# Optimization experiments

Measured on AMD Instinct MI355X. Metric: run time of the kernel, lower is better.

## Reference

```python
import jax, jax.numpy as jnp
import numpy as np

SOS_TOKEN = 0


def setup_inputs() -> dict:
    B, T, V, E, H = 128, 512, 1024, 256, 512
    key = jax.random.key(0)
    ks = jax.random.split(key, 11)
    return {
        "encoder_outputs": jax.random.normal(ks[0], (B, 8, H), jnp.float32),
        "enc_h": jax.random.normal(ks[1], (2, B, H), jnp.float32),
        "enc_c": jax.random.normal(ks[2], (2, B, H), jnp.float32),
        "target_tensor": jax.random.randint(ks[3], (B, T), 0, V, jnp.int64 if jax.config.jax_enable_x64 else jnp.int32),
        "embedding": jax.random.normal(ks[4], (V, E), jnp.float32) * 0.02,
        "W_ih": jax.random.normal(ks[5], (4 * H, E), jnp.float32) * 0.05,
        "W_hh": jax.random.normal(ks[6], (4 * H, H), jnp.float32) * 0.05,
        "b_ih": jax.random.normal(ks[7], (4 * H,), jnp.float32) * 0.05,
        "b_hh": jax.random.normal(ks[8], (4 * H,), jnp.float32) * 0.05,
        "W_out": jax.random.normal(ks[9], (V, H), jnp.float32) * 0.05,
        "b_out": jax.random.normal(ks[10], (V,), jnp.float32) * 0.05,
    }


def reference(encoder_outputs, enc_h, enc_c, target_tensor, embedding,
              W_ih, W_hh, b_ih, b_hh, W_out, b_out):
    B = encoder_outputs.shape[0]
    H = W_hh.shape[1]
    # decoder initial state: mean over encoder layer dim -> (B, H)
    h0 = enc_h.mean(axis=0)
    c0 = enc_c.mean(axis=0)
    # teacher-forced input tokens: [SOS, y_0, ..., y_{T-2}]  -> (B, T)
    sos = jnp.full((B, 1), SOS_TOKEN, dtype=target_tensor.dtype)
    tokens = jnp.concatenate([sos, target_tensor[:, :-1]], axis=1)
    # embed + relu, then precompute all input-side gate projections: (B, T, 4H)
    x = jax.nn.relu(embedding[tokens])
    gates_x = jnp.einsum("bte,ge->btg", x, W_ih) + b_ih + b_hh

    def lstm_step(carry, gx):
        h, c = carry  # (B, H) each; gx: (B, 4H)
        gates = gx + h @ W_hh.T
        i, f, g, o = jnp.split(gates, 4, axis=-1)  # torch gate order i,f,g,o
        c = jax.nn.sigmoid(f) * c + jax.nn.sigmoid(i) * jnp.tanh(g)
        h = jax.nn.sigmoid(o) * jnp.tanh(c)
        return (h, c), h

    (h_T, c_T), hs = jax.lax.scan(lstm_step, (h0, c0), gates_x.transpose(1, 0, 2))
    hs = hs.transpose(1, 0, 2)  # (B, T, H)
    logits = jnp.einsum("bth,vh->btv", hs, W_out) + b_out
    log_probs = jax.nn.log_softmax(logits, axis=-1)
    # final hidden mirrors torch's (num_layers=1, B, H) layout
    return log_probs, h_T[None], c_T[None]
```

## Files before the change

### kernel.cpp

```cpp
#include <hip/hip_runtime.h>

typedef unsigned short u16;
typedef unsigned int u32;
typedef unsigned long long u64;
typedef short bf16x8 __attribute__((ext_vector_type(8)));
typedef float f32x4 __attribute__((ext_vector_type(4)));
typedef unsigned u32x4 __attribute__((ext_vector_type(4)));

#define NB 128
#define NT 512
#define NV 1024
#define NE 256
#define NH 512
#define NG 2048

#define POISON64 0xFFFFFFFFFFFFFFFFULL
#define POISON32 0xFFFFFFFFu
#define HEX_T 65536
#define PROBE_CYCLES 480000ULL

__device__ __forceinline__ u16 f2bf(float f) {
  union { float f; unsigned u; } v; v.f = f;
  unsigned r = v.u + 0x7FFFu + ((v.u >> 16) & 1u);
  return (u16)(r >> 16);
}
__device__ __forceinline__ float bf2f(u16 u) {
  union { unsigned u; float f; } v; v.u = ((unsigned)u) << 16;
  return v.f;
}
__device__ __forceinline__ float sigm(float x) { return 1.f / (1.f + __expf(-x)); }
__device__ __forceinline__ float tanh_f(float x) {
  x = fminf(fmaxf(x, -20.f), 20.f);
  float e = __expf(2.f * x);
  return (e - 1.f) / (e + 1.f);
}
__device__ __forceinline__ u64 memtime() {
  u64 t;
  asm volatile("s_memtime %0\n\ts_waitcnt lgkmcnt(0)" : "=s"(t));
  return t;
}

#define MFMA16(a, b, c) __builtin_amdgcn_mfma_f32_16x16x32_bf16((a), (b), (c), 0, 0, 0)

__device__ __forceinline__ uint2 pf_load_u64(const void* p) {
  uint2 r;
  asm volatile("global_load_dwordx2 %0, %1, off" : "=v"(r) : "v"(p) : "memory");
  return r;
}
__device__ __forceinline__ void ex_store(u16* p, u64 v) {
  (void)__hip_atomic_exchange((u64*)p, v, __ATOMIC_RELAXED, __HIP_MEMORY_SCOPE_AGENT);
}
__device__ __forceinline__ void ex_load2(const u16* p, bool fast, u32x4& q0, u32x4& q1) {
  if (fast) {
    asm volatile(
        "global_load_dwordx4 %0, %2, off sc0\n\t"
        "global_load_dwordx4 %1, %3, off sc0\n\t"
        "s_waitcnt vmcnt(0)"
        : "=&v"(q0), "=&v"(q1)
        : "v"(p), "v"(p + 8)
        : "memory");
  } else {
    asm volatile(
        "global_load_dwordx4 %0, %2, off sc0 sc1\n\t"
        "global_load_dwordx4 %1, %3, off sc0 sc1\n\t"
        "s_waitcnt vmcnt(0)"
        : "=&v"(q0), "=&v"(q1)
        : "v"(p), "v"(p + 8)
        : "memory");
  }
}

__device__ __forceinline__ void stage_h(const u16* hexg, u16* HsBuf, int tid, bool fast) {
  const u16* p = hexg + (size_t)tid * 16;
  u32x4 q0, q1;
  ex_load2(p, fast, q0, q1);
  for (;;) {
    u64 a = (u64)q0.x | ((u64)q0.y << 32), b = (u64)q0.z | ((u64)q0.w << 32);
    u64 c = (u64)q1.x | ((u64)q1.y << 32), d = (u64)q1.z | ((u64)q1.w << 32);
    if (!((a == POISON64) | (b == POISON64) | (c == POISON64) | (d == POISON64))) break;
    ex_load2(p, fast, q0, q1);
  }
  int s2 = tid >> 5, b = (tid >> 1) & 15, half = tid & 1;
  int K0 = s2 * 4 + half * 2;
  *(u32x4*)&HsBuf[b * 512 + ((K0 ^ (b & 7)) << 3)] = q0;
  *(u32x4*)&HsBuf[b * 512 + (((K0 + 1) ^ (b & 7)) << 3)] = q1;
}

__device__ __forceinline__ void group_setup(u32* ctrl, u32* disc_lds, int* fast_shp,
                                            int bid, int tid, int& g, int& s, bool& fast) {
  u32* disc = ctrl; u32* probe = ctrl + 128; u32* ready2 = ctrl + 256; u32* demote = ctrl + 384;
  int w = tid >> 6, lane = tid & 63;
  if (tid == 0) {
    u32 xcd;
    asm volatile("s_getreg_b32 %0, hwreg(HW_REG_XCC_ID)" : "=s"(xcd));
    __hip_atomic_store(&disc[bid], xcd & 7u, __ATOMIC_RELAXED, __HIP_MEMORY_SCOPE_AGENT);
  }
  if (w == 0) {
    const u64* d64 = (const u64*)disc;
    u64 v;
    do { v = __hip_atomic_load(&d64[lane], __ATOMIC_RELAXED, __HIP_MEMORY_SCOPE_AGENT); }
    while ((u32)v == POISON32 || (u32)(v >> 32) == POISON32);
    disc_lds[2 * lane] = (u32)v; disc_lds[2 * lane + 1] = (u32)(v >> 32);
  }
  __syncthreads();
  u64 cnt64 = 0;
  for (int i = 0; i < 128; ++i) cnt64 += 1ULL << ((disc_lds[i] & 7) * 8);
  int myx = (int)(disc_lds[bid] & 7);
  int rank = 0;
  for (int i = 0; i < bid; ++i) if ((int)(disc_lds[i] & 7) == myx) rank++;
  int pre = 0;
  for (int x = 0; x < myx; ++x) pre += (int)((cnt64 >> (x * 8)) & 255);
  int pos = pre + rank;
  g = pos >> 4; s = pos & 15;
  fast = false;
  { int p0 = 0;
    for (int x = 0; x < 8; ++x) { int c = (int)((cnt64 >> (x * 8)) & 255);
      if (p0 <= g * 16 && g * 16 + 16 <= p0 + c) fast = true; p0 += c; } }
  if (fast) {
    if (tid == 0)
      (void)__hip_atomic_exchange(&probe[g * 16 + s], 1u, __ATOMIC_RELAXED,
                                  __HIP_MEMORY_SCOPE_AGENT);
    if (w == 0) {
      bool to = false;
      if (lane < 16) {
        u32 pv = POISON32;
        u64 t0 = memtime();
        for (;;) {
          asm volatile("global_load_dword %0, %1, off sc0\n\ts_waitcnt vmcnt(0)"
                       : "=v"(pv) : "v"(&probe[g * 16 + lane]) : "memory");
          if (pv != POISON32) break;
          if (memtime() - t0 > PROBE_CYCLES) break;
        }
        to = (pv == POISON32);
      }
      if (__any(to) && lane == 0) {
        __hip_atomic_store(&demote[g], 1u, __ATOMIC_RELAXED, __HIP_MEMORY_SCOPE_AGENT);
        asm volatile("s_waitcnt vmcnt(0)" ::: "memory");
      }
    }
    __syncthreads();
    if (tid == 0)
      __hip_atomic_store(&ready2[g * 16 + s], 1u, __ATOMIC_RELAXED, __HIP_MEMORY_SCOPE_AGENT);
    if (w == 0 && lane < 16) {
      u32 rv;
      do { rv = __hip_atomic_load(&ready2[g * 16 + lane], __ATOMIC_RELAXED, __HIP_MEMORY_SCOPE_AGENT); }
      while (rv == POISON32);
    }
    if (tid == 0)
      *fast_shp = (int)(__hip_atomic_load(&demote[g], __ATOMIC_RELAXED, __HIP_MEMORY_SCOPE_AGENT) == 0u);
    __syncthreads();
    fast = (*fast_shp != 0);
  }
}

__global__ __launch_bounds__(256) void prep_kernel(
    const float* __restrict__ enc_h, const float* __restrict__ W_ih,
    const float* __restrict__ W_hh, const float* __restrict__ b_ih,
    const float* __restrict__ b_hh, const float* __restrict__ W_out,
    u16* __restrict__ wih_p, u16* __restrict__ whh_p, u16* __restrict__ wout_b,
    float* __restrict__ bias_p, u16* __restrict__ hex, u32* __restrict__ ctrl) {
  int idx = blockIdx.x * 256 + threadIdx.x;
  int stride = gridDim.x * 256;
  if (idx < 128) { ctrl[idx] = POISON32; ctrl[128 + idx] = POISON32; ctrl[256 + idx] = POISON32; }
  if (idx < 8) ctrl[384 + idx] = 0;
  const int N0 = NG * NE, N1 = NG * NH, N2 = NV * NH, N3 = NG, N4 = NB * NH;
  int total = N0 + N1 + N2 + N3 + N4;
  for (int i = idx; i < total; i += stride) {
    int j = i;
    if (j < N0) {
      int r = j >> 8, k = j & 255;
      int orig = (r & 3) * NH + (r >> 2);
      wih_p[j] = f2bf(W_ih[orig * NE + k]);
    } else if ((j -= N0) < N1) {
      int r = j >> 9, k = j & 511;
      int orig = (r & 3) * NH + (r >> 2);
      whh_p[j] = f2bf(W_hh[orig * NH + k]);
    } else if ((j -= N1) < N2) {
      wout_b[j] = f2bf(W_out[j]);
    } else if ((j -= N2) < N3) {
      int orig = (j & 3) * NH + (j >> 2);
      bias_p[j] = b_ih[orig] + b_hh[orig];
    } else {
      j -= N3;
      int bb = j >> 9, jj = j & 511;
      float v = 0.5f * (enc_h[j] + enc_h[N4 + j]);
      hex[((size_t)(bb >> 4) * 16 + (jj >> 5)) * 512 + (size_t)(bb & 15) * 32 + (jj & 31)] = f2bf(v);
    }
  }
  u64* hp = (u64*)(hex + HEX_T);
  const int NP = NT * (HEX_T / 4);
  for (int i = idx; i < NP; i += stride) hp[i] = POISON64;
}

__global__ __launch_bounds__(256) void gates_kernel(
    const int* __restrict__ target, const float* __restrict__ emb,
    const u16* __restrict__ wih_p, const float* __restrict__ bias_p,
    u16* __restrict__ gates) {
  __shared__ __align__(16) u16 As[NB * NE];
  int t = blockIdx.y, nTile = blockIdx.x, tid = threadIdx.x;
  for (int i = tid; i < NB * 64; i += 256) {
    int row = i >> 6, c = i & 63;
    int tok = (t == 0) ? 0 : target[row * NT + t - 1];
    float4 f = *(const float4*)(emb + (size_t)tok * NE + c * 4);
    ushort4 pk = make_ushort4(f2bf(fmaxf(f.x, 0.f)), f2bf(fmaxf(f.y, 0.f)),
                              f2bf(fmaxf(f.z, 0.f)), f2bf(fmaxf(f.w, 0.f)));
    int g = c >> 1;
    int off = row * NE + ((((g ^ (row & 7)) << 3)) | ((c & 1) << 2));
    *(ushort4*)&As[off] = pk;
  }
  __syncthreads();
  int w = tid >> 6, lane = tid & 63, l15 = lane & 15, l4 = lane >> 4;
  int mOff = (w & 1) * 64, nOff = (w >> 1) * 64;
  f32x4 acc[4][4] = {};
  for (int kk = 0; kk < 8; ++kk) {
    bf16x8 a[4], bb[4];
    for (int fm = 0; fm < 4; ++fm) {
      int row = mOff + fm * 16 + l15;
      a[fm] = *(const bf16x8*)&As[row * NE + (((kk * 4 + l4) ^ (row & 7)) << 3)];
    }
    int k0 = kk * 32 + l4 * 8;
    for (int fn = 0; fn < 4; ++fn) {
      int n = nTile * 128 + nOff + fn * 16 + l15;
      bb[fn] = *(const bf16x8*)(wih_p + (size_t)n * NE + k0);
    }
    for (int fm = 0; fm < 4; ++fm)
      for (int fn = 0; fn < 4; ++fn)
        acc[fm][fn] = MFMA16(a[fm], bb[fn], acc[fm][fn]);
  }
  for (int fn = 0; fn < 4; ++fn) {
    int n = nTile * 128 + nOff + fn * 16 + l15;
    float bias = bias_p[n];
    for (int fm = 0; fm < 4; ++fm)
      for (int i2 = 0; i2 < 4; ++i2) {
        int row = mOff + fm * 16 + l4 * 4 + i2;
        gates[((size_t)t * NB + row) * NG + n] = f2bf(acc[fm][fn][i2] + bias);
      }
  }
}

__global__ __launch_bounds__(512, 1) void lstm_kernel(
    const float* __restrict__ enc_c, const u16* __restrict__ gates,
    const u16* __restrict__ whh_p, u16* __restrict__ hex,
    float* __restrict__ out_tail, u32* __restrict__ ctrl) {
  __shared__ __align__(16) u16 Hs[2][16 * 512];
  __shared__ u32 disc_lds[128];
  __shared__ int fast_sh;
  int bid = blockIdx.x, tid = threadIdx.x;
  int w = tid >> 6, lane = tid & 63, l15 = lane & 15, l4 = lane >> 4;
  int g, s; bool fast;
  group_setup(ctrl, disc_lds, &fast_sh, bid, tid, g, s, fast);

  bf16x8 wreg[16];
  {
    const u16* wp = whh_p + (size_t)(s * 128 + w * 16 + l15) * NH + l4 * 8;
#pragma unroll
    for (int kk = 0; kk < 16; ++kk) {
      wreg[kk] = *(const bf16x8*)(wp + kk * 32);
      asm volatile("" : "+v"(wreg[kk]));
    }
  }
  int b = g * 16 + l15;
  int j = s * 32 + w * 4 + l4;
  float creg = 0.5f * (enc_c[b * NH + j] + enc_c[NB * NH + b * NH + j]);
  uint2 pg = pf_load_u64(gates + (size_t)b * NG + s * 128 + w * 16 + l4 * 4);
  stage_h(hex + (size_t)g * 8192, &Hs[0][0], tid, fast);
  __syncthreads();
  int cur = 0;

  for (int t = 0; t < NT; ++t) {
    asm volatile("s_waitcnt vmcnt(0)" ::: "memory");
    __builtin_amdgcn_sched_barrier(0);
    f32x4 acc;
    acc[0] = bf2f((u16)(pg.x & 0xFFFF));
    acc[1] = bf2f((u16)(pg.x >> 16));
    acc[2] = bf2f((u16)(pg.y & 0xFFFF));
    acc[3] = bf2f((u16)(pg.y >> 16));
    if (t + 1 < NT)
      pg = pf_load_u64(gates + ((size_t)(t + 1) * NB + b) * NG + s * 128 + w * 16 + l4 * 4);
#pragma unroll
    for (int kk = 0; kk < 16; ++kk) {
      bf16x8 hv = *(const bf16x8*)&Hs[cur][l15 * 512 + (((kk * 4 + l4) ^ (l15 & 7)) << 3)];
      acc = MFMA16(wreg[kk], hv, acc);
    }
    float ig = sigm(acc[0]);
    float fg = sigm(acc[1]);
    float gg = tanh_f(acc[2]);
    float og = sigm(acc[3]);
    float cn = fg * creg + ig * gg;
    creg = cn;
    float hn = og * tanh_f(cn);
    {
      u32 v = (u32)f2bf(hn);
      u32 v2 = (u32)__shfl_xor((int)v, 16, 64);
      v = v | (v2 << 16);
      u32 hi = (u32)__shfl_xor((int)v, 32, 64);
      if (l4 == 0) {
        u64 qv = (u64)v | ((u64)hi << 32);
        u16* hdst = hex + ((size_t)(t + 1) * 8 + g) * 8192;
        ex_store(hdst + ((size_t)s * 16 + l15) * 32 + w * 4, qv);
      }
    }
    if (t == NT - 1) {
      out_tail[b * NH + j] = hn;
      out_tail[NB * NH + b * NH + j] = cn;
      break;
    }
    stage_h(hex + ((size_t)(t + 1) * 8 + g) * 8192, &Hs[cur ^ 1][0], tid, fast);
    __syncthreads();
    cur ^= 1;
  }
}

__global__ __launch_bounds__(256) void logits_kernel(
    const u16* __restrict__ hex, const u16* __restrict__ wout_b,
    const float* __restrict__ b_out, float* __restrict__ out) {
  int tt = blockIdx.y, nTile = blockIdx.x;
  int tid = threadIdx.x, w = tid >> 6, lane = tid & 63, l15 = lane & 15, l4 = lane >> 4;
  int mOff = (w & 1) * 64, nOff = (w >> 1) * 64;
  const u16* A = hex + (size_t)(tt + 1) * HEX_T;
  f32x4 acc[4][4] = {};
  for (int kk = 0; kk < 16; ++kk) {
    int k0 = kk * 32 + l4 * 8;
    bf16x8 a[4], bb[4];
#pragma unroll
    for (int fm = 0; fm < 4; ++fm) {
      int gg = (mOff >> 4) + fm;
      a[fm] = *(const bf16x8*)(A + ((size_t)gg * 16 + kk) * 512 + l15 * 32 + l4 * 8);
    }
#pragma unroll
    for (int fn = 0; fn < 4; ++fn) {
      int v = nTile * 128 + nOff + fn * 16 + l15;
      bb[fn] = *(const bf16x8*)(wout_b + (size_t)v * NH + k0);
    }
    for (int fm = 0; fm < 4; ++fm)
      for (int fn = 0; fn < 4; ++fn)
        acc[fm][fn] = MFMA16(a[fm], bb[fn], acc[fm][fn]);
  }
  for (int fn = 0; fn < 4; ++fn) {
    int v = nTile * 128 + nOff + fn * 16 + l15;
    float bias = b_out[v];
    for (int fm = 0; fm < 4; ++fm)
      for (int i2 = 0; i2 < 4; ++i2) {
        int brow = mOff + fm * 16 + l4 * 4 + i2;
        out[((size_t)brow * NT + tt) * NV + v] = acc[fm][fn][i2] + bias;
      }
  }
}

__global__ __launch_bounds__(256) void lsm_kernel(float* __restrict__ out) {
  int row = blockIdx.x * 4 + (threadIdx.x >> 6);
  int lane = threadIdx.x & 63;
  float* p = out + (size_t)row * NV + lane * 4;
  float4 x[4];
  float m = -1e30f;
#pragma unroll
  for (int i = 0; i < 4; ++i) {
    x[i] = *(const float4*)(p + i * 256);
    m = fmaxf(m, fmaxf(fmaxf(x[i].x, x[i].y), fmaxf(x[i].z, x[i].w)));
  }
#pragma unroll
  for (int o = 1; o < 64; o <<= 1) m = fmaxf(m, __shfl_xor(m, o, 64));
  float s = 0.f;
#pragma unroll
  for (int i = 0; i < 4; ++i)
    s += __expf(x[i].x - m) + __expf(x[i].y - m) + __expf(x[i].z - m) + __expf(x[i].w - m);
#pragma unroll
  for (int o = 1; o < 64; o <<= 1) s += __shfl_xor(s, o, 64);
  float lse = m + __logf(s);
#pragma unroll
  for (int i = 0; i < 4; ++i) {
    float4 y = x[i];
    y.x -= lse; y.y -= lse; y.z -= lse; y.w -= lse;
    *(float4*)(p + i * 256) = y;
  }
}

extern "C" void kernel_launch(void* const* d_in, const int* in_sizes, int n_in,
                              void* d_out, int out_size, void* d_ws, size_t ws_size,
                              hipStream_t stream) {
  (void)in_sizes; (void)n_in; (void)out_size; (void)ws_size;
  const float* enc_h  = (const float*)d_in[1];
  const float* enc_c  = (const float*)d_in[2];
  const int*   target = (const int*)d_in[3];
  const float* emb    = (const float*)d_in[4];
  const float* W_ih   = (const float*)d_in[5];
  const float* W_hh   = (const float*)d_in[6];
  const float* b_ih   = (const float*)d_in[7];
  const float* b_hh   = (const float*)d_in[8];
  const float* W_out  = (const float*)d_in[9];
  const float* b_out  = (const float*)d_in[10];

  char* ws = (char*)d_ws;
  u16*   wih_p  = (u16*)(ws);
  u16*   whh_p  = (u16*)(ws + (1 << 20));
  u16*   wout_b = (u16*)(ws + (3 << 20));
  float* bias_p = (float*)(ws + (4 << 20));
  u32*   ctrl   = (u32*)(ws + (4 << 20) + 8192);
  u16*   hex    = (u16*)(ws + (4 << 20) + 16384);

  u16*   gates  = (u16*)d_out;
  float* out    = (float*)d_out;
  float* out_tail = out + (size_t)NB * NT * NV;

  prep_kernel<<<dim3(2048), 256, 0, stream>>>(enc_h, W_ih, W_hh, b_ih, b_hh, W_out,
                                              wih_p, whh_p, wout_b, bias_p, hex, ctrl);
  gates_kernel<<<dim3(16, 512), 256, 0, stream>>>(target, emb, wih_p, bias_p, gates);
  {
    const float* enc_c_a = enc_c;
    const u16* gates_a = gates;
    const u16* whh_a = whh_p;
    u16* hex_a = hex;
    float* tail_a = out_tail;
    u32* ctrl_a = ctrl;
    void* args[] = {&enc_c_a, &gates_a, &whh_a, &hex_a, &tail_a, &ctrl_a};
    hipLaunchCooperativeKernel((const void*)lstm_kernel, dim3(128), dim3(512),
                               args, 0, stream);
  }
  logits_kernel<<<dim3(8, 512), 256, 0, stream>>>(hex, wout_b, b_out, out);
  lsm_kernel<<<16384, 256, 0, stream>>>(out);
}
```

Baseline: 4.032 ms.

## Fuse logits GEMM into cooperative LSTM kernel, overlapping via hidden-state polling

```diff
diff --git a/kernel.cpp b/kernel.cpp
--- a/kernel.cpp
+++ b/kernel.cpp
@@ -42,6 +42,9 @@
 
 #define MFMA16(a, b, c) __builtin_amdgcn_mfma_f32_16x16x32_bf16((a), (b), (c), 0, 0, 0)
 
+__device__ __forceinline__ u64 dc_load_u64(const void* p) {
+  return __hip_atomic_load((const u64*)p, __ATOMIC_RELAXED, __HIP_MEMORY_SCOPE_AGENT);
+}
 __device__ __forceinline__ uint2 pf_load_u64(const void* p) {
   uint2 r;
   asm volatile("global_load_dwordx2 %0, %1, off" : "=v"(r) : "v"(p) : "memory");
@@ -84,6 +87,16 @@
   int K0 = s2 * 4 + half * 2;
   *(u32x4*)&HsBuf[b * 512 + ((K0 ^ (b & 7)) << 3)] = q0;
   *(u32x4*)&HsBuf[b * 512 + (((K0 + 1) ^ (b & 7)) << 3)] = q1;
+}
+
+__device__ __forceinline__ bf16x8 w_poll_frag(const u16* p) {
+  u64 lo = dc_load_u64(p), hi = dc_load_u64(p + 4);
+  while (lo == POISON64 || hi == POISON64) {
+    asm volatile("s_sleep 64");
+    lo = dc_load_u64(p); hi = dc_load_u64(p + 4);
+  }
+  u32x4 q = {(u32)lo, (u32)(lo >> 32), (u32)hi, (u32)(hi >> 32)};
+  return __builtin_bit_cast(bf16x8, q);
 }
 
 __device__ __forceinline__ void group_setup(u32* ctrl, u32* disc_lds, int* fast_shp,
@@ -233,117 +246,132 @@
     for (int fm = 0; fm < 4; ++fm)
       for (int i2 = 0; i2 < 4; ++i2) {
         int row = mOff + fm * 16 + l4 * 4 + i2;
-        gates[((size_t)t * NB + row) * NG + n] = f2bf(acc[fm][fn][i2] + bias);
-      }
-  }
-}
-
-__global__ __launch_bounds__(512, 1) void lstm_kernel(
+        gates[((size_t)row * NT + t) * NG + n] = f2bf(acc[fm][fn][i2] + bias);
+      }
+  }
+}
+
+__global__ __launch_bounds__(512, 2) void mega_kernel(
     const float* __restrict__ enc_c, const u16* __restrict__ gates,
     const u16* __restrict__ whh_p, u16* __restrict__ hex,
-    float* __restrict__ out_tail, u32* __restrict__ ctrl) {
+    float* __restrict__ out_tail, u32* __restrict__ ctrl,
+    const u16* __restrict__ wout_b, const float* __restrict__ b_out,
+    float* __restrict__ out) {
   __shared__ __align__(16) u16 Hs[2][16 * 512];
   __shared__ u32 disc_lds[128];
   __shared__ int fast_sh;
   int bid = blockIdx.x, tid = threadIdx.x;
   int w = tid >> 6, lane = tid & 63, l15 = lane & 15, l4 = lane >> 4;
-  int g, s; bool fast;
-  group_setup(ctrl, disc_lds, &fast_sh, bid, tid, g, s, fast);
-
-  bf16x8 wreg[16];
-  {
-    const u16* wp = whh_p + (size_t)(s * 128 + w * 16 + l15) * NH + l4 * 8;
-#pragma unroll
-    for (int kk = 0; kk < 16; ++kk) {
-      wreg[kk] = *(const bf16x8*)(wp + kk * 32);
-      asm volatile("" : "+v"(wreg[kk]));
-    }
-  }
-  int b = g * 16 + l15;
-  int j = s * 32 + w * 4 + l4;
-  float creg = 0.5f * (enc_c[b * NH + j] + enc_c[NB * NH + b * NH + j]);
-  uint2 pg = pf_load_u64(gates + (size_t)b * NG + s * 128 + w * 16 + l4 * 4);
-  stage_h(hex + (size_t)g * 8192, &Hs[0][0], tid, fast);
-  __syncthreads();
-  int cur = 0;
-
-  for (int t = 0; t < NT; ++t) {
-    asm volatile("s_waitcnt vmcnt(0)" ::: "memory");
-    __builtin_amdgcn_sched_barrier(0);
-    f32x4 acc;
-    acc[0] = bf2f((u16)(pg.x & 0xFFFF));
-    acc[1] = bf2f((u16)(pg.x >> 16));
-    acc[2] = bf2f((u16)(pg.y & 0xFFFF));
-    acc[3] = bf2f((u16)(pg.y >> 16));
-    if (t + 1 < NT)
-      pg = pf_load_u64(gates + ((size_t)(t + 1) * NB + b) * NG + s * 128 + w * 16 + l4 * 4);
-#pragma unroll
-    for (int kk = 0; kk < 16; ++kk) {
-      bf16x8 hv = *(const bf16x8*)&Hs[cur][l15 * 512 + (((kk * 4 + l4) ^ (l15 & 7)) << 3)];
-      acc = MFMA16(wreg[kk], hv, acc);
-    }
-    float ig = sigm(acc[0]);
-    float fg = sigm(acc[1]);
-    float gg = tanh_f(acc[2]);
-    float og = sigm(acc[3]);
-    float cn = fg * creg + ig * gg;
-    creg = cn;
-    float hn = og * tanh_f(cn);
+
+  if (bid < 128) {
+    int g, s; bool fast;
+    group_setup(ctrl, disc_lds, &fast_sh, bid, tid, g, s, fast);
+
+    bf16x8 wreg[16];
     {
-      u32 v = (u32)f2bf(hn);
-      u32 v2 = (u32)__shfl_xor((int)v, 16, 64);
-      v = v | (v2 << 16);
-      u32 hi = (u32)__shfl_xor((int)v, 32, 64);
-      if (l4 == 0) {
-        u64 qv = (u64)v | ((u64)hi << 32);
-        u16* hdst = hex + ((size_t)(t + 1) * 8 + g) * 8192;
-        ex_store(hdst + ((size_t)s * 16 + l15) * 32 + w * 4, qv);
-      }
-    }
-    if (t == NT - 1) {
-      out_tail[b * NH + j] = hn;
-      out_tail[NB * NH + b * NH + j] = cn;
-      break;
-    }
-    stage_h(hex + ((size_t)(t + 1) * 8 + g) * 8192, &Hs[cur ^ 1][0], tid, fast);
+      const u16* wp = whh_p + (size_t)(s * 128 + w * 16 + l15) * NH + l4 * 8;
+#pragma unroll
+      for (int kk = 0; kk < 16; ++kk) {
+        wreg[kk] = *(const bf16x8*)(wp + kk * 32);
+        asm volatile("" : "+v"(wreg[kk]));
+      }
+    }
+    int b = g * 16 + l15;
+    int j = s * 32 + w * 4 + l4;
+    float creg = 0.5f * (enc_c[b * NH + j] + enc_c[NB * NH + b * NH + j]);
+    uint2 pg = pf_load_u64(gates + ((size_t)b * NT + 0) * NG + s * 128 + w * 16 + l4 * 4);
+    stage_h(hex + (size_t)g * 8192, &Hs[0][0], tid, fast);
     __syncthreads();
-    cur ^= 1;
-  }
-}
-
-__global__ __launch_bounds__(256) void logits_kernel(
-    const u16* __restrict__ hex, const u16* __restrict__ wout_b,
-    const float* __restrict__ b_out, float* __restrict__ out) {
-  int tt = blockIdx.y, nTile = blockIdx.x;
-  int tid = threadIdx.x, w = tid >> 6, lane = tid & 63, l15 = lane & 15, l4 = lane >> 4;
-  int mOff = (w & 1) * 64, nOff = (w >> 1) * 64;
-  const u16* A = hex + (size_t)(tt + 1) * HEX_T;
-  f32x4 acc[4][4] = {};
-  for (int kk = 0; kk < 16; ++kk) {
-    int k0 = kk * 32 + l4 * 8;
-    bf16x8 a[4], bb[4];
-#pragma unroll
-    for (int fm = 0; fm < 4; ++fm) {
-      int gg = (mOff >> 4) + fm;
-      a[fm] = *(const bf16x8*)(A + ((size_t)gg * 16 + kk) * 512 + l15 * 32 + l4 * 8);
-    }
-#pragma unroll
-    for (int fn = 0; fn < 4; ++fn) {
-      int v = nTile * 128 + nOff + fn * 16 + l15;
-      bb[fn] = *(const bf16x8*)(wout_b + (size_t)v * NH + k0);
-    }
-    for (int fm = 0; fm < 4; ++fm)
-      for (int fn = 0; fn < 4; ++fn)
-        acc[fm][fn] = MFMA16(a[fm], bb[fn], acc[fm][fn]);
-  }
-  for (int fn = 0; fn < 4; ++fn) {
-    int v = nTile * 128 + nOff + fn * 16 + l15;
-    float bias = b_out[v];
-    for (int fm = 0; fm < 4; ++fm)
-      for (int i2 = 0; i2 < 4; ++i2) {
-        int brow = mOff + fm * 16 + l4 * 4 + i2;
-        out[((size_t)brow * NT + tt) * NV + v] = acc[fm][fn][i2] + bias;
-      }
+    int cur = 0;
+
+    for (int t = 0; t < NT; ++t) {
+      asm volatile("s_waitcnt vmcnt(0)" ::: "memory");
+      __builtin_amdgcn_sched_barrier(0);
+      f32x4 acc;
+      acc[0] = bf2f((u16)(pg.x & 0xFFFF));
+      acc[1] = bf2f((u16)(pg.x >> 16));
+      acc[2] = bf2f((u16)(pg.y & 0xFFFF));
+      acc[3] = bf2f((u16)(pg.y >> 16));
+      if (t + 1 < NT)
+        pg = pf_load_u64(gates + ((size_t)b * NT + (t + 1)) * NG + s * 128 + w * 16 + l4 * 4);
+#pragma unroll
+      for (int kk = 0; kk < 16; ++kk) {
+        bf16x8 hv = *(const bf16x8*)&Hs[cur][l15 * 512 + (((kk * 4 + l4) ^ (l15 & 7)) << 3)];
+        acc = MFMA16(wreg[kk], hv, acc);
+      }
+      float ig = sigm(acc[0]);
+      float fg = sigm(acc[1]);
+      float gg = tanh_f(acc[2]);
+      float og = sigm(acc[3]);
+      float cn = fg * creg + ig * gg;
+      creg = cn;
+      float hn = og * tanh_f(cn);
+      {
+        u32 v = (u32)f2bf(hn);
+        u32 v2 = (u32)__shfl_xor((int)v, 16, 64);
+        v = v | (v2 << 16);
+        u32 hi = (u32)__shfl_xor((int)v, 32, 64);
+        if (l4 == 0) {
+          u64 qv = (u64)v | ((u64)hi << 32);
+          u16* hdst = hex + ((size_t)(t + 1) * 8 + g) * 8192;
+          ex_store(hdst + ((size_t)s * 16 + l15) * 32 + w * 4, qv);
+        }
+      }
+      if (t == NT - 1) {
+        out_tail[b * NH + j] = hn;
+        out_tail[NB * NH + b * NH + j] = cn;
+        break;
+      }
+      stage_h(hex + ((size_t)(t + 1) * 8 + g) * 8192, &Hs[cur ^ 1][0], tid, fast);
+      __syncthreads();
+      cur ^= 1;
+    }
+  } else {
+    int wid = bid - 128;
+#pragma unroll 1
+    for (int rep = 0; rep < 4; ++rep) {
+      int tt = wid + rep * 128;
+      const u16* A = hex + (size_t)(tt + 1) * HEX_T;
+#pragma unroll 1
+      for (int mh = 0; mh < 2; ++mh) {
+        f32x4 acc[2][4][4] = {};
+#pragma unroll 1
+        for (int kk = 0; kk < 16; ++kk) {
+          bf16x8 a[4];
+#pragma unroll
+          for (int fm = 0; fm < 4; ++fm)
+            a[fm] = w_poll_frag(A + (((size_t)(mh * 4 + fm) * 16 + kk) * 512 + l15 * 32 + l4 * 8));
+          bf16x8 bb[2][4];
+#pragma unroll
+          for (int np = 0; np < 2; ++np)
+#pragma unroll
+            for (int fn = 0; fn < 4; ++fn)
+              bb[np][fn] = *(const bf16x8*)(wout_b +
+                  (size_t)(np * 512 + w * 64 + fn * 16 + l15) * NH + kk * 32 + l4 * 8);
+#pragma unroll
+          for (int np = 0; np < 2; ++np)
+#pragma unroll
+            for (int fm = 0; fm < 4; ++fm)
+#pragma unroll
+              for (int fn = 0; fn < 4; ++fn)
+                acc[np][fm][fn] = MFMA16(a[fm], bb[np][fn], acc[np][fm][fn]);
+        }
+#pragma unroll
+        for (int np = 0; np < 2; ++np)
+#pragma unroll
+          for (int fn = 0; fn < 4; ++fn) {
+            int v = np * 512 + w * 64 + fn * 16 + l15;
+            float bias = b_out[v];
+#pragma unroll
+            for (int fm = 0; fm < 4; ++fm)
+#pragma unroll
+              for (int i2 = 0; i2 < 4; ++i2) {
+                int m = mh * 64 + fm * 16 + l4 * 4 + i2;
+                out[((size_t)m * NT + tt) * NV + v] = acc[np][fm][fn][i2] + bias;
+              }
+          }
+      }
+    }
   }
 }
 
@@ -412,10 +440,13 @@
     u16* hex_a = hex;
     float* tail_a = out_tail;
     u32* ctrl_a = ctrl;
-    void* args[] = {&enc_c_a, &gates_a, &whh_a, &hex_a, &tail_a, &ctrl_a};
-    hipLaunchCooperativeKernel((const void*)lstm_kernel, dim3(128), dim3(512),
+    const u16* woutb_a = wout_b;
+    const float* bout_a = b_out;
+    float* out_a = out;
+    void* args[] = {&enc_c_a, &gates_a, &whh_a, &hex_a, &tail_a, &ctrl_a,
+                    &woutb_a, &bout_a, &out_a};
+    hipLaunchCooperativeKernel((const void*)mega_kernel, dim3(256), dim3(512),
                                args, 0, stream);
   }
-  logits_kernel<<<dim3(8, 512), 256, 0, stream>>>(hex, wout_b, b_out, out);
   lsm_kernel<<<16384, 256, 0, stream>>>(out);
 }
```

After: 3.987 ms. About the same (-1.1%).
